# Kernel optimization log

Hardware: AMD Instinct MI355X
Metric: run time of the kernel (lower is better)

The kernel has to match this reference:

```python
import jax, jax.numpy as jnp
import numpy as np
from jax import lax

P_LEN, Q_LEN, B = 400, 60, 128
P_IN, Q_IN, H = 512, 512, 256
D = P_IN + Q_IN  # gate / GRU input size


def setup_inputs() -> dict:
    key = jax.random.key(0)
    ks = jax.random.split(key, 10)
    s = 0.05  # small init scale to keep tanh/sigmoid in sane range
    return {
        "q_input": jax.random.normal(ks[0], (Q_LEN, B, Q_IN), jnp.float32),
        "p_input": jax.random.normal(ks[1], (P_LEN, B, P_IN), jnp.float32),
        "q_mask": jnp.zeros((Q_LEN, B), dtype=bool),
        "Wq": jax.random.normal(ks[2], (2, Q_IN, H), jnp.float32) * s,
        "Wp": jax.random.normal(ks[3], (2, P_IN, H), jnp.float32) * s,
        "Ws": jax.random.normal(ks[4], (2, H, H), jnp.float32) * s,
        "v": jax.random.normal(ks[5], (2, H, 1), jnp.float32) * s,
        "gate_W": jax.random.normal(ks[6], (2, D, D), jnp.float32) * s,
        "gate_b": jnp.zeros((2, D), jnp.float32),
        "gru_Wih": jax.random.normal(ks[7], (2, 3 * H, D), jnp.float32) * s,
        "gru_Whh": jax.random.normal(ks[8], (2, 3 * H, H), jnp.float32) * s,
        "gru_bih": jnp.zeros((2, 3 * H), jnp.float32),
        "gru_bhh": jnp.zeros((2, 3 * H), jnp.float32),
    }


def _run_direction(q_input, p_input, q_mask, Wq, Wp, Ws, v,
                   gate_W, gate_b, gru_Wih, gru_Whh, gru_bih, gru_bhh,
                   reverse):
    # q_input: [Q, B, q_in], p_input: [P, B, p_in], q_mask: [Q, B] bool
    hid = Ws.shape[1]
    q_temp = jnp.einsum('qbe,eh->qbh', q_input, Wq)  # precomputed once, [Q,B,H]
    p_temp = jnp.einsum('pbe,eh->pbh', p_input, Wp)  # [P,B,H]
    mask = q_mask[:, :, None]                        # [Q,B,1]

    def step(state, xs):
        p_x, p_t = xs  # [B,p_in], [B,H]
        state_temp = state @ Ws                                   # [B,H]
        logits = jnp.tanh(q_temp + p_t[None] + state_temp[None]) @ v  # [Q,B,1]
        logits = jnp.where(mask, -jnp.inf, logits)
        weights = jax.nn.softmax(logits, axis=0)                  # over q_len
        att = jnp.sum(weights * q_input, axis=0)                  # [B,q_in]
        x = jnp.concatenate([p_x, att], axis=-1)                  # [B,D]
        x = x * jax.nn.sigmoid(x @ gate_W.T + gate_b)             # Gate
        # torch GRUCell math
        gi = x @ gru_Wih.T + gru_bih
        gh = state @ gru_Whh.T + gru_bhh
        i_r, i_z, i_n = jnp.split(gi, 3, axis=-1)
        h_r, h_z, h_n = jnp.split(gh, 3, axis=-1)
        r = jax.nn.sigmoid(i_r + h_r)
        z = jax.nn.sigmoid(i_z + h_z)
        n = jnp.tanh(i_n + r * h_n)
        new_state = (1.0 - z) * n + z * state
        return new_state, new_state

    init = jnp.zeros((p_input.shape[1], hid), p_input.dtype)
    _, out = lax.scan(step, init, (p_input, p_temp), reverse=reverse)
    return out  # [P,B,H], already in original time order (scan reverse handles it)


def reference(q_input, p_input, q_mask, Wq, Wp, Ws, v, gate_W, gate_b,
              gru_Wih, gru_Whh, gru_bih, gru_bhh):
    out_fw = _run_direction(q_input, p_input, q_mask, Wq[0], Wp[0], Ws[0], v[0],
                            gate_W[0], gate_b[0], gru_Wih[0], gru_Whh[0],
                            gru_bih[0], gru_bhh[0], reverse=False)
    out_bw = _run_direction(q_input, p_input, q_mask, Wq[1], Wp[1], Ws[1], v[1],
                            gate_W[1], gate_b[1], gru_Wih[1], gru_Whh[1],
                            gru_bih[1], gru_bhh[1], reverse=True)
    return jnp.concatenate([out_fw, out_bw], axis=-1)  # [P,B,2H]
```

## Files before the change

### kernel.cpp

```cpp
#include <hip/hip_runtime.h>

#define PL 400
#define QL 60
#define BB 128
#define EE 512
#define HH 256
#define DD 1024
#define G3 768
#define NBLK 256
#define NTHR 512
#define LDK 72

typedef __attribute__((ext_vector_type(8))) short bfrag;
typedef __attribute__((ext_vector_type(4))) float facc;
typedef __attribute__((ext_vector_type(4))) unsigned uintx4;
typedef __attribute__((ext_vector_type(4))) unsigned short ushortx4;

__device__ __forceinline__ unsigned short f2bf(float x) {
  unsigned u = __float_as_uint(x);
  return (unsigned short)((u + 0x7fffu + ((u >> 16) & 1u)) >> 16);
}
__device__ __forceinline__ float bf2f(unsigned short h) {
  return __uint_as_float(((unsigned)h) << 16);
}
__device__ __forceinline__ void split_bf(float x, unsigned short& hi, unsigned short& lo) {
  hi = f2bf(x);
  lo = f2bf(x - bf2f(hi));
}
__device__ __forceinline__ unsigned packf(float x) {
  unsigned short hi, lo;
  split_bf(x, hi, lo);
  return ((unsigned)hi << 16) | lo;
}
__device__ __forceinline__ float unpk(unsigned p) {
  return bf2f((unsigned short)(p >> 16)) + bf2f((unsigned short)(p & 0xffffu));
}
__device__ __forceinline__ float sigm(float x) {
  return __builtin_amdgcn_rcpf(1.f + __expf(-x));
}
__device__ __forceinline__ float ftanh(float x) {
  float xc = fminf(fmaxf(x, -10.f), 10.f);
  float t = __expf(2.f * xc);
  return (t - 1.f) * __builtin_amdgcn_rcpf(t + 1.f);
}

__device__ __forceinline__ float ald(const float* p) {
  return __hip_atomic_load((float*)p, __ATOMIC_RELAXED, __HIP_MEMORY_SCOPE_AGENT);
}
__device__ __forceinline__ void ast(float* p, float v) {
  __hip_atomic_store(p, v, __ATOMIC_RELAXED, __HIP_MEMORY_SCOPE_AGENT);
}
__device__ __forceinline__ unsigned aldu(const unsigned* p) {
  return __hip_atomic_load((unsigned*)p, __ATOMIC_RELAXED, __HIP_MEMORY_SCOPE_AGENT);
}
__device__ __forceinline__ void astu(unsigned* p, unsigned v) {
  __hip_atomic_store(p, v, __ATOMIC_RELAXED, __HIP_MEMORY_SCOPE_AGENT);
}
__device__ __forceinline__ unsigned long long aldull(const unsigned long long* p) {
  return __hip_atomic_load((unsigned long long*)p, __ATOMIC_RELAXED, __HIP_MEMORY_SCOPE_AGENT);
}
__device__ __forceinline__ void pollge(unsigned* f, unsigned tgt) {
  unsigned sp = 0;
  while (aldu(f) < tgt) {
    __builtin_amdgcn_s_sleep(1);
    if (++sp > (1u << 26)) break;
  }
}

constexpr size_t SZ_PT  = (size_t)2 * PL * BB * HH;
constexpr size_t SZ_GIP = (size_t)2 * 4 * BB * G3;
constexpr size_t SZ_GHP = (size_t)2 * BB * G3;
constexpr size_t SZ_WST = (size_t)2 * HH * HH;
constexpr size_t OFF_PT  = 0;
constexpr size_t OFF_GIP = OFF_PT + SZ_PT;
constexpr size_t OFF_GHP = OFF_GIP + SZ_GIP;
constexpr size_t OFF_WST = OFF_GHP + SZ_GHP;
constexpr size_t F32_TOT = OFF_WST + SZ_WST;
constexpr size_t UOFF_ATTP  = 0;
constexpr size_t UOFF_XPACK = UOFF_ATTP + (size_t)2 * 2 * BB * EE;
constexpr size_t UOFF_HPACK = UOFF_XPACK + (size_t)2 * 2 * BB * DD;
constexpr size_t U_TOT      = UOFF_HPACK + (size_t)2 * BB * HH;
constexpr size_t HSZ_WQT = (size_t)2 * HH * EE;
constexpr size_t HSZ_GW  = (size_t)2 * DD * DD;
constexpr size_t HSZ_WIH = (size_t)2 * G3 * DD;
constexpr size_t HSZ_WHH = (size_t)2 * G3 * HH;
constexpr size_t HOFF_WQTH = 0;
constexpr size_t HOFF_WQTL = HOFF_WQTH + HSZ_WQT;
constexpr size_t HOFF_WPTH = HOFF_WQTL + HSZ_WQT;
constexpr size_t HOFF_WPTL = HOFF_WPTH + HSZ_WQT;
constexpr size_t HOFF_GWH  = HOFF_WPTL + HSZ_WQT;
constexpr size_t HOFF_GWL  = HOFF_GWH + HSZ_GW;
constexpr size_t HOFF_WIHH = HOFF_GWL + HSZ_GW;
constexpr size_t HOFF_WIHL = HOFF_WIHH + HSZ_WIH;
constexpr size_t HOFF_WHHH = HOFF_WIHL + HSZ_WIH;
constexpr size_t HOFF_WHHL = HOFF_WHHH + HSZ_WHH;
constexpr size_t HOFF_QIN16 = HOFF_WHHL + HSZ_WHH;
constexpr size_t HOFF_QT16  = HOFF_QIN16 + (size_t)QL * BB * EE;
constexpr size_t H_TOT      = HOFF_QT16 + (size_t)2 * QL * BB * HH;

#define FA 0
#define FG 256
#define FI 320
#define FH 416
#define FC 440

__device__ __forceinline__ void gbar(unsigned* slots, unsigned gen) {
  asm volatile("" ::: "memory");
  __syncthreads();
  if (threadIdx.x == 0)
    __hip_atomic_store(&slots[blockIdx.x], gen, __ATOMIC_RELAXED, __HIP_MEMORY_SCOPE_AGENT);
  if (threadIdx.x < NBLK) pollge(&slots[threadIdx.x], gen);
  __syncthreads();
  asm volatile("" ::: "memory");
}

template <int NT, bool BSPLIT, int NCH, int ASRC>
__device__ void gemm_direct(facc* acc,
                            const unsigned short* wh, const unsigned short* wl,
                            const unsigned* apk, const float* a32, int as,
                            int kbase, int wchbase) {
  const int tid = threadIdx.x;
  const int lane = tid & 63;
  const int w = tid >> 6;
  constexpr int FN = NT / 16;
  const int lr = lane & 15;
  const int lk = (lane >> 4) << 3;
  const int row = (w << 4) + lr;

#pragma unroll 2
  for (int ch = 0; ch < NCH; ++ch) {
    const int kk = kbase + (ch << 6);
#pragma unroll
    for (int k32 = 0; k32 < 64; k32 += 32) {
      const int ko = kk + k32 + lk;
      bfrag ah, al_;
      {
        unsigned hu[4], lu[4];
        if constexpr (ASRC == 0) {
          const unsigned long long* src =
              (const unsigned long long*)(apk + (size_t)row * as + ko);
          unsigned long long d0 = aldull(src + 0);
          unsigned long long d1 = aldull(src + 1);
          unsigned long long d2 = aldull(src + 2);
          unsigned long long d3 = aldull(src + 3);
          unsigned p0 = (unsigned)d0, p1 = (unsigned)(d0 >> 32);
          unsigned p2 = (unsigned)d1, p3 = (unsigned)(d1 >> 32);
          unsigned p4 = (unsigned)d2, p5 = (unsigned)(d2 >> 32);
          unsigned p6 = (unsigned)d3, p7 = (unsigned)(d3 >> 32);
          hu[0] = (p0 >> 16) | (p1 & 0xffff0000u);  lu[0] = (p0 & 0xffffu) | (p1 << 16);
          hu[1] = (p2 >> 16) | (p3 & 0xffff0000u);  lu[1] = (p2 & 0xffffu) | (p3 << 16);
          hu[2] = (p4 >> 16) | (p5 & 0xffff0000u);  lu[2] = (p4 & 0xffffu) | (p5 << 16);
          hu[3] = (p6 >> 16) | (p7 & 0xffff0000u);  lu[3] = (p6 & 0xffffu) | (p7 << 16);
        } else {
          const float* src = a32 + (size_t)row * as + ko;
          float4 v0 = *(const float4*)src;
          float4 v1 = *(const float4*)(src + 4);
          unsigned short h0, l0, h1, l1;
          split_bf(v0.x, h0, l0); split_bf(v0.y, h1, l1);
          hu[0] = h0 | ((unsigned)h1 << 16); lu[0] = l0 | ((unsigned)l1 << 16);
          split_bf(v0.z, h0, l0); split_bf(v0.w, h1, l1);
          hu[1] = h0 | ((unsigned)h1 << 16); lu[1] = l0 | ((unsigned)l1 << 16);
          split_bf(v1.x, h0, l0); split_bf(v1.y, h1, l1);
          hu[2] = h0 | ((unsigned)h1 << 16); lu[2] = l0 | ((unsigned)l1 << 16);
          split_bf(v1.z, h0, l0); split_bf(v1.w, h1, l1);
          hu[3] = h0 | ((unsigned)h1 << 16); lu[3] = l0 | ((unsigned)l1 << 16);
        }
        uintx4 hv = {hu[0], hu[1], hu[2], hu[3]};
        uintx4 lv = {lu[0], lu[1], lu[2], lu[3]};
        ah  = __builtin_bit_cast(bfrag, hv);
        al_ = __builtin_bit_cast(bfrag, lv);
      }
      bfrag bhf[FN], blf[FN];
#pragma unroll
      for (int f = 0; f < FN; f++) {
        const int bo = ((wchbase + ch) * NT + (f << 4) + lr) * LDK + k32 + lk;
        bhf[f] = *(const bfrag*)&wh[bo];
        if constexpr (BSPLIT) blf[f] = *(const bfrag*)&wl[bo];
      }
#pragma unroll
      for (int j = 0; j < FN; j++) {
        acc[j] = __builtin_amdgcn_mfma_f32_16x16x32_bf16(al_, bhf[j], acc[j], 0, 0, 0);
        if constexpr (BSPLIT)
          acc[j] = __builtin_amdgcn_mfma_f32_16x16x32_bf16(ah, blf[j], acc[j], 0, 0, 0);
        acc[j] = __builtin_amdgcn_mfma_f32_16x16x32_bf16(ah, bhf[j], acc[j], 0, 0, 0);
      }
    }
  }
}

__device__ void gemm_pro(unsigned short* sAh, unsigned short* sAl, unsigned short* warea,
                         const float* a32,
                         const unsigned short* bh_g, const unsigned short* bl_g,
                         float* dstf, unsigned short* dst16) {
  const int tid = threadIdx.x;
  const int lane = tid & 63;
  const int w = tid >> 6;
  const int wm = (w >> 2) << 6;
  const int wn = (w & 3) << 5;
  const int lr = lane & 15;
  const int lk = (lane >> 4) << 3;
  unsigned short* wh = warea;
  unsigned short* wl = warea + 128 * LDK;
  const facc fz = {0.f, 0.f, 0.f, 0.f};
  facc acc[4][2];
#pragma unroll
  for (int i = 0; i < 4; i++)
#pragma unroll
    for (int j = 0; j < 2; j++) acc[i][j] = fz;
  for (int ch = 0; ch < 8; ++ch) {
    const int kk0 = ch << 6;
    for (int i = tid; i < 8192; i += NTHR) {
      const int r = i >> 6, k = i & 63;
      unsigned short uh, ul;
      split_bf(a32[(size_t)r * EE + kk0 + k], uh, ul);
      sAh[r * LDK + k] = uh;
      sAl[r * LDK + k] = ul;
      wh[r * LDK + k] = bh_g[(size_t)r * EE + kk0 + k];
      wl[r * LDK + k] = bl_g[(size_t)r * EE + kk0 + k];
    }
    __syncthreads();
#pragma unroll
    for (int k32 = 0; k32 < 64; k32 += 32) {
      bfrag ah[4], al_[4], bhf[2], blf[2];
#pragma unroll
      for (int f = 0; f < 4; f++) {
        const int ao = (wm + (f << 4) + lr) * LDK + k32 + lk;
        ah[f]  = *(const bfrag*)&sAh[ao];
        al_[f] = *(const bfrag*)&sAl[ao];
      }
#pragma unroll
      for (int f = 0; f < 2; f++) {
        const int bo = (wn + (f << 4) + lr) * LDK + k32 + lk;
        bhf[f] = *(const bfrag*)&wh[bo];
        blf[f] = *(const bfrag*)&wl[bo];
      }
#pragma unroll
      for (int i = 0; i < 4; i++)
#pragma unroll
        for (int j = 0; j < 2; j++) {
          acc[i][j] = __builtin_amdgcn_mfma_f32_16x16x32_bf16(al_[i], bhf[j], acc[i][j], 0, 0, 0);
          acc[i][j] = __builtin_amdgcn_mfma_f32_16x16x32_bf16(ah[i], blf[j], acc[i][j], 0, 0, 0);
          acc[i][j] = __builtin_amdgcn_mfma_f32_16x16x32_bf16(ah[i], bhf[j], acc[i][j], 0, 0, 0);
        }
    }
    __syncthreads();
  }
  const int orow = (lane >> 4) << 2;
  const int ocol = lane & 15;
#pragma unroll
  for (int i = 0; i < 4; i++)
#pragma unroll
    for (int j = 0; j < 2; j++)
#pragma unroll
      for (int q = 0; q < 4; q++) {
        const size_t o = (size_t)(wm + (i << 4) + orow + q) * HH + (wn + (j << 4) + ocol);
        if (dstf) dstf[o] = acc[i][j][q];
        else dst16[o] = f2bf(acc[i][j][q]);
      }
}

__global__ void __launch_bounds__(256) k_transpose_qp(
    const float* __restrict__ Wq, const float* __restrict__ Wp,
    unsigned short* __restrict__ wqth, unsigned short* __restrict__ wqtl,
    unsigned short* __restrict__ wpth, unsigned short* __restrict__ wptl) {
  __shared__ float tile[64 * 65];
  const int blk = blockIdx.x;
  const int mat = blk >> 6;
  const int rem = blk & 63;
  const int d = rem >> 5;
  const int rem2 = rem & 31;
  const int kt = rem2 >> 2;
  const int nt = rem2 & 3;
  const float* src = mat ? Wp : Wq;
  unsigned short* dh = mat ? wpth : wqth;
  unsigned short* dl = mat ? wptl : wqtl;
  const int tid = threadIdx.x;
  for (int i = tid; i < 4096; i += 256) {
    int kr = i >> 6, nc = i & 63;
    tile[kr * 65 + nc] = src[((size_t)d * EE + kt * 64 + kr) * HH + nt * 64 + nc];
  }
  __syncthreads();
  for (int i = tid; i < 4096; i += 256) {
    int n = i >> 6, k = i & 63;
    unsigned short hi, lo;
    split_bf(tile[k * 65 + n], hi, lo);
    size_t o = ((size_t)d * HH + nt * 64 + n) * EE + kt * 64 + k;
    dh[o] = hi; dl[o] = lo;
  }
}

__global__ void __launch_bounds__(256) k_split_w(
    const float* __restrict__ gw, const float* __restrict__ wih, const float* __restrict__ whh,
    unsigned short* __restrict__ gwh, unsigned short* __restrict__ gwl,
    unsigned short* __restrict__ wihh, unsigned short* __restrict__ wihl,
    unsigned short* __restrict__ whhh, unsigned short* __restrict__ whhl) {
  const size_t N1 = HSZ_GW, N2 = HSZ_WIH, N3 = HSZ_WHH;
  for (size_t i = (size_t)blockIdx.x * 256 + threadIdx.x; i < N1 + N2 + N3;
       i += (size_t)gridDim.x * 256) {
    float x; unsigned short *ph, *pl; size_t o;
    if (i < N1)           { o = i;           x = gw[o];  ph = gwh;  pl = gwl; }
    else if (i < N1 + N2) { o = i - N1;      x = wih[o]; ph = wihh; pl = wihl; }
    else                  { o = i - N1 - N2; x = whh[o]; ph = whhh; pl = whhl; }
    unsigned short hi, lo;
    split_bf(x, hi, lo);
    ph[o] = hi; pl[o] = lo;
  }
}

__global__ void __launch_bounds__(256) k_wst_qin(const float* __restrict__ Ws,
                                                 float* __restrict__ wst,
                                                 const float* __restrict__ qin,
                                                 unsigned short* __restrict__ qin16) {
  const size_t NQ = (size_t)QL * BB * EE;
  for (size_t i = (size_t)blockIdx.x * 256 + threadIdx.x; i < SZ_WST + NQ;
       i += (size_t)gridDim.x * 256) {
    if (i < SZ_WST) {
      int d = (int)(i >> 16);
      int j = (int)((i >> 8) & 255);
      int k = (int)(i & 255);
      wst[i] = Ws[((size_t)d * HH + k) * HH + j];
    } else {
      size_t o = i - SZ_WST;
      qin16[o] = f2bf(qin[o]);
    }
  }
}

__global__ void __launch_bounds__(NTHR, 1) pe_main(
    const float* __restrict__ qin, const float* __restrict__ pin,
    const unsigned char* __restrict__ qmask,
    const float* __restrict__ vvec, const float* __restrict__ gateb,
    const float* __restrict__ bih, const float* __restrict__ bhh,
    float* __restrict__ out,
    float* __restrict__ fws, unsigned* __restrict__ upck,
    unsigned short* __restrict__ hws, unsigned* __restrict__ bar) {
  __shared__ __align__(16) unsigned short smem[56320];
  unsigned short* sAh = smem;
  unsigned short* sAl = smem + 9216;
  unsigned short* warea = smem + 18432;
  float* fsm = (float*)smem;
  float* sv_perm   = (float*)(smem + 55296);
  float* sstv_perm = (float*)(smem + 55808);

  float* pt   = fws + OFF_PT;
  float* gip  = fws + OFF_GIP;
  float* ghp  = fws + OFF_GHP;
  float* wst  = fws + OFF_WST;
  unsigned* attp0 = upck + UOFF_ATTP;
  unsigned* xpck0 = upck + UOFF_XPACK;
  unsigned* hpack = upck + UOFF_HPACK;
  unsigned short* wqth = hws + HOFF_WQTH;
  unsigned short* wqtl = hws + HOFF_WQTL;
  unsigned short* wpth = hws + HOFF_WPTH;
  unsigned short* wptl = hws + HOFF_WPTL;
  unsigned short* gwh  = hws + HOFF_GWH;
  unsigned short* wihh = hws + HOFF_WIHH;
  unsigned short* wihl = hws + HOFF_WIHL;
  unsigned short* whhh = hws + HOFF_WHHH;
  unsigned short* whhl = hws + HOFF_WHHL;
  const unsigned short* qin16 = hws + HOFF_QIN16;
  unsigned short* qt16 = hws + HOFF_QT16;
  unsigned* flg = bar + 256;

  const int blk = blockIdx.x;
  const int tid = threadIdx.x;
  const int lane = tid & 63;
  const int w = tid >> 6;

  const bool isGate = (blk < 64);
  const bool isGi   = (blk >= 64 && blk < 160);
  const bool isGh   = (blk >= 160 && blk < 184);
  const int gd = blk >> 5, gct = blk & 31, coloff = gct * 32;
  const int gi_g = blk - 64, id_ = gi_g / 48, ir = gi_g % 48;
  const int int_ = ir >> 2, iks = ir & 3;
  const int gh_g = blk - 160, hd = gh_g / 12, hnt = gh_g % 12;

  for (int tt = blk; tt < 1840; tt += NBLK) {
    if (tt < 1600) {
      int d = tt / 800, rem = tt % 800, mt = rem >> 1, ntp = rem & 1;
      gemm_pro(sAh, sAl, warea, pin + (size_t)mt * BB * EE,
               wpth + ((size_t)d * HH + ntp * 128) * EE,
               wptl + ((size_t)d * HH + ntp * 128) * EE,
               pt + ((size_t)d * PL * BB + (size_t)mt * BB) * HH + ntp * 128, nullptr);
    } else {
      int u2 = tt - 1600;
      int d = u2 / 120, rem = u2 % 120, mt = rem >> 1, ntp = rem & 1;
      gemm_pro(sAh, sAl, warea, qin + (size_t)mt * BB * EE,
               wqth + ((size_t)d * HH + ntp * 128) * EE,
               wqtl + ((size_t)d * HH + ntp * 128) * EE,
               nullptr,
               qt16 + ((size_t)d * QL * BB + (size_t)mt * BB) * HH + ntp * 128);
    }
  }

  if (isGate) {
    const unsigned short* src = gwh + (size_t)(gd * DD + coloff) * DD;
    for (int i = tid; i < 32768; i += NTHR) {
      int ch = i >> 11, n = (i >> 6) & 31, k = i & 63;
      warea[(ch * 32 + n) * LDK + k] = src[(size_t)n * DD + ch * 64 + k];
    }
  } else if (isGi) {
    const unsigned short* sh = wihh + (size_t)(id_ * G3 + int_ * 64) * DD + iks * 256;
    const unsigned short* sl = wihl + (size_t)(id_ * G3 + int_ * 64) * DD + iks * 256;
    for (int i = tid; i < 16384; i += NTHR) {
      int ch = i >> 12, n = (i >> 6) & 63, k = i & 63;
      warea[(ch * 64 + n) * LDK + k]         = sh[(size_t)n * DD + ch * 64 + k];
      warea[18432 + (ch * 64 + n) * LDK + k] = sl[(size_t)n * DD + ch * 64 + k];
    }
  } else if (isGh) {
    const unsigned short* sh = whhh + (size_t)(hd * G3 + hnt * 64) * HH;
    const unsigned short* sl = whhl + (size_t)(hd * G3 + hnt * 64) * HH;
    for (int i = tid; i < 16384; i += NTHR) {
      int ch = i >> 12, n = (i >> 6) & 63, k = i & 63;
      warea[(ch * 64 + n) * LDK + k]         = sh[(size_t)n * HH + ch * 64 + k];
      warea[18432 + (ch * 64 + n) * LDK + k] = sl[(size_t)n * HH + ch * 64 + k];
    }
  }

  __builtin_amdgcn_fence(__ATOMIC_RELEASE, "agent");
  gbar(bar, 1);

  const int d_ab = blk >> 7, b_ab = blk & 127;
  if (tid < 256) {
    sv_perm[tid] = vvec[d_ab * HH + tid];
    sstv_perm[tid] = 0.f;
  }
  const bool qmv = (tid < 64 && lane < QL) ? (qmask[lane * BB + b_ab] != 0) : false;
  __syncthreads();

  facc pinacc[2];
  if (isGate) {
    const facc fz = {0.f, 0.f, 0.f, 0.f};
    pinacc[0] = fz; pinacc[1] = fz;
    const int t0 = gd ? (PL - 1) : 0;
    gemm_direct<32, false, 8, 1>(pinacc, warea, nullptr,
                                 nullptr, pin + (size_t)t0 * BB * EE, EE, 0, 0);
  }

  float hreg = 0.f;
  float* sm = fsm;
  float* slog = fsm + 512;
  float* swgt = fsm + 576;
  float* spart = fsm + 896;
  float* hrow = fsm + 1408;

  for (int s = 0; s < PL; ++s) {
    const int par = s & 1;
    unsigned* attp = attp0 + (size_t)par * 2 * BB * EE;
    unsigned* xpack = xpck0 + (size_t)par * 2 * BB * DD;
    const unsigned gen = (unsigned)(s + 1);

    {
      const int d = d_ab, b = b_ab;
      const int t = d ? (PL - 1 - s) : s;
      if (tid < 256) {
        float ptv = __builtin_nontemporal_load(&pt[(((size_t)d * PL + t) * BB + b) * HH + tid]);
        sm[tid] = sstv_perm[tid] + ptv;
      }
      __syncthreads();
      {
        const int j4 = lane << 2;
        const float4 smv = *(const float4*)&sm[j4];
        const float4 svv = *(const float4*)&sv_perm[j4];
        for (int q = w; q < QL; q += 8) {
          const unsigned short* qrow = qt16 + (((size_t)d * QL + q) * BB + b) * HH;
          ushortx4 qv = *(const ushortx4*)&qrow[j4];
          float a = ftanh(bf2f(qv.x) + smv.x) * svv.x
                  + ftanh(bf2f(qv.y) + smv.y) * svv.y
                  + ftanh(bf2f(qv.z) + smv.z) * svv.z
                  + ftanh(bf2f(qv.w) + smv.w) * svv.w;
          for (int off = 32; off; off >>= 1) a += __shfl_down(a, off, 64);
          if (lane == 0) slog[q] = a;
        }
      }
      __syncthreads();
      if (tid < 64) {
        float x = -3.0e38f;
        if (lane < QL) {
          x = slog[lane];
          if (qmv) x = -3.0e38f;
        }
        float mx = x;
        for (int off = 32; off; off >>= 1) mx = fmaxf(mx, __shfl_xor(mx, off, 64));
        float e = (lane < QL) ? __expf(x - mx) : 0.f;
        float sum2 = e;
        for (int off = 32; off; off >>= 1) sum2 += __shfl_xor(sum2, off, 64);
        if (lane < QL) swgt[lane] = e * __builtin_amdgcn_rcpf(sum2);
      }
      __syncthreads();
      {
        const int c = tid;
        float a0 = 0.f, a1 = 0.f, a2 = 0.f, a3 = 0.f;
        const unsigned short* qb = qin16 + (size_t)b * EE + c;
        for (int q = 0; q < QL; q += 4) {
          a0 += swgt[q]     * bf2f(qb[(size_t)q * BB * EE]);
          a1 += swgt[q + 1] * bf2f(qb[(size_t)(q + 1) * BB * EE]);
          a2 += swgt[q + 2] * bf2f(qb[(size_t)(q + 2) * BB * EE]);
          a3 += swgt[q + 3] * bf2f(qb[(size_t)(q + 3) * BB * EE]);
        }
        astu(&attp[((size_t)d * BB + b) * EE + c], packf((a0 + a1) + (a2 + a3)));
      }
      __syncthreads();
      if (tid == 0) astu(&flg[FA + d_ab * 128 + b_ab], gen);
    }

    const int orow = (lane >> 4) << 2;
    const int ocol = lane & 15;
    const int rbase = w << 4;

    if (isGate) {
      if (tid < 128) pollge(&flg[FA + gd * 128 + tid], gen);
      __syncthreads();
      gemm_direct<32, false, 8, 0>(pinacc, warea, nullptr,
                                   attp + (size_t)gd * BB * EE, nullptr, EE, 0, 8);
      {
        const int t = gd ? (PL - 1 - s) : s;
        const float* pin_t = pin + (size_t)t * BB * EE;
#pragma unroll
        for (int i = 0; i < 2; i++)
#pragma unroll
          for (int q = 0; q < 4; q++) {
            const int row = rbase + orow + q;
            const int gcol = coloff + (i << 4) + ocol;
            float uv = (gct < 16) ? pin_t[(size_t)row * EE + gcol]
                                  : unpk(aldu(&attp[((size_t)gd * BB + row) * EE + gcol - EE]));
            float x = uv * sigm(pinacc[i][q] + gateb[(size_t)gd * DD + gcol]);
            astu(&xpack[((size_t)gd * BB + row) * DD + gcol], packf(x));
          }
      }
      __syncthreads();
      if (tid == 0) astu(&flg[FG + gd * 32 + gct], gen);
      if (s + 1 < PL) {
        const facc fz = {0.f, 0.f, 0.f, 0.f};
        pinacc[0] = fz; pinacc[1] = fz;
        const int t2 = gd ? (PL - 2 - s) : (s + 1);
        gemm_direct<32, false, 8, 1>(pinacc, warea, nullptr,
                                     nullptr, pin + (size_t)t2 * BB * EE, EE, 0, 0);
      }
    } else if (isGi) {
      if (tid < 8) pollge(&flg[FG + id_ * 32 + iks * 8 + tid], gen);
      __syncthreads();
      const facc fz = {0.f, 0.f, 0.f, 0.f};
      facc acc[4] = {fz, fz, fz, fz};
      gemm_direct<64, true, 4, 0>(acc, warea, warea + 18432,
                                  xpack + (size_t)id_ * BB * DD, nullptr, DD, iks * 256, 0);
#pragma unroll
      for (int j = 0; j < 4; j++)
#pragma unroll
        for (int q = 0; q < 4; q++) {
          const int row = rbase + orow + q;
          const int col = int_ * 64 + (j << 4) + ocol;
          ast(&gip[((size_t)(id_ * 4 + iks) * BB + row) * G3 + col], acc[j][q]);
        }
      __syncthreads();
      if (tid == 0) astu(&flg[FI + id_ * 48 + ir], gen);
    } else if (isGh) {
      if (s > 0 && tid < 128) pollge(&flg[FC + hd * 128 + tid], (unsigned)s);
      __syncthreads();
      const facc fz = {0.f, 0.f, 0.f, 0.f};
      facc acc[4] = {fz, fz, fz, fz};
      gemm_direct<64, true, 4, 0>(acc, warea, warea + 18432,
                                  hpack + (size_t)hd * BB * HH, nullptr, HH, 0, 0);
#pragma unroll
      for (int j = 0; j < 4; j++)
#pragma unroll
        for (int q = 0; q < 4; q++) {
          const int row = rbase + orow + q;
          const int col = hnt * 64 + (j << 4) + ocol;
          ast(&ghp[((size_t)hd * BB + row) * G3 + col], acc[j][q]);
        }
      __syncthreads();
      if (tid == 0) astu(&flg[FH + hd * 12 + hnt], gen);
    }

    {
      if (tid < 48) pollge(&flg[FI + d_ab * 48 + tid], gen);
      else if (tid < 60) pollge(&flg[FH + d_ab * 12 + (tid - 48)], gen);
      __syncthreads();
      const int d = d_ab, b = b_ab;
      const int j = tid & 255, half = tid >> 8;
      const int t = d ? (PL - 1 - s) : s;
      const size_t rb = (size_t)d * BB + b;
      float gi3[3], gh3[3];
#pragma unroll
      for (int c3 = 0; c3 < 3; c3++) {
        float acc2 = bih[(size_t)d * G3 + c3 * HH + j];
#pragma unroll
        for (int ks = 0; ks < 4; ks++)
          acc2 += ald(&gip[((size_t)(d * 4 + ks) * BB + b) * G3 + c3 * HH + j]);
        gi3[c3] = acc2;
        gh3[c3] = ald(&ghp[rb * G3 + c3 * HH + j]) + bhh[(size_t)d * G3 + c3 * HH + j];
      }
      float r = sigm(gi3[0] + gh3[0]);
      float z = sigm(gi3[1] + gh3[1]);
      float n = ftanh(gi3[2] + r * gh3[2]);
      float hn = (1.f - z) * n + z * hreg;
      hreg = hn;
      if (half == 0) {
        __builtin_nontemporal_store(hn, &out[((size_t)t * BB + b) * 512 + d * HH + j]);
        astu(&hpack[rb * HH + j], packf(hn));
        hrow[j] = hn;
      }
      __syncthreads();
      if (tid == 0) astu(&flg[FC + d_ab * 128 + b_ab], gen);
      float part = 0.f;
      const float* wr = wst + ((size_t)d * HH + j) * HH + (half << 7);
      const float* hr = hrow + (half << 7);
#pragma unroll
      for (int k = 0; k < 128; k += 4) {
        float4 w4 = *(const float4*)&wr[k];
        float4 h4 = *(const float4*)&hr[k];
        part += w4.x * h4.x + w4.y * h4.y + w4.z * h4.z + w4.w * h4.w;
      }
      spart[tid] = part;
      __syncthreads();
      if (tid < 256) sstv_perm[tid] = spart[tid] + spart[tid + 256];
      __syncthreads();
    }
  }
}

extern "C" void kernel_launch(void* const* d_in, const int* in_sizes, int n_in,
                              void* d_out, int out_size, void* d_ws, size_t ws_size,
                              hipStream_t stream) {
  const float* qin = (const float*)d_in[0];
  const float* pin = (const float*)d_in[1];
  const unsigned char* qmask = (const unsigned char*)d_in[2];
  const float* Wq  = (const float*)d_in[3];
  const float* Wp  = (const float*)d_in[4];
  const float* Ws  = (const float*)d_in[5];
  const float* v   = (const float*)d_in[6];
  const float* gw  = (const float*)d_in[7];
  const float* gb  = (const float*)d_in[8];
  const float* wih = (const float*)d_in[9];
  const float* whh = (const float*)d_in[10];
  const float* bih = (const float*)d_in[11];
  const float* bhh = (const float*)d_in[12];
  float* out = (float*)d_out;

  char* base = (char*)d_ws;
  float* fws = (float*)base;
  unsigned* upck = (unsigned*)(base + F32_TOT * sizeof(float));
  unsigned short* hws = (unsigned short*)(base + F32_TOT * sizeof(float) + U_TOT * sizeof(unsigned));
  unsigned* bar = (unsigned*)(base + F32_TOT * sizeof(float) + U_TOT * sizeof(unsigned) +
                              H_TOT * sizeof(unsigned short));
  size_t need = F32_TOT * sizeof(float) + U_TOT * sizeof(unsigned) +
                H_TOT * sizeof(unsigned short) + 8192;
  if (ws_size < need) return;

  hipMemsetAsync(upck + UOFF_HPACK, 0, (size_t)2 * BB * HH * sizeof(unsigned), stream);
  hipMemsetAsync(bar, 0, 4096, stream);

  k_transpose_qp<<<128, 256, 0, stream>>>(Wq, Wp,
      hws + HOFF_WQTH, hws + HOFF_WQTL, hws + HOFF_WPTH, hws + HOFF_WPTL);
  k_split_w<<<1024, 256, 0, stream>>>(gw, wih, whh,
      hws + HOFF_GWH, hws + HOFF_GWL, hws + HOFF_WIHH, hws + HOFF_WIHL,
      hws + HOFF_WHHH, hws + HOFF_WHHL);
  k_wst_qin<<<2048, 256, 0, stream>>>(Ws, fws + OFF_WST, qin,
                                      hws + HOFF_QIN16);
  pe_main<<<NBLK, NTHR, 0, stream>>>(qin, pin, qmask, v, gb, bih, bhh, out,
                                     fws, upck, hws, bar);
}
```

Measured before the change: 24.87 ms.

## Drop A-low MFMA pass in gate GEMM and cache q_temp slice in LDS

Adds an ASPLIT template flag so the gate GEMM uses only the bf16-high part of the activation. This removes one of the two MFMAs per fragment plus the low-part unpacking, while the GI/GH GEMMs keep full split precision. It also copies each block's q_temp slice (QL x H bf16) into extra LDS once, so the per-step attention logits read it from shared memory instead of global memory. Gate accuracy drops somewhat, and the larger LDS footprint could matter for occupancy, though there is only one block per CU here.

```diff
diff --git a/kernel.cpp b/kernel.cpp
--- a/kernel.cpp
+++ b/kernel.cpp
@@ -114,7 +114,7 @@
   asm volatile("" ::: "memory");
 }
 
-template <int NT, bool BSPLIT, int NCH, int ASRC>
+template <int NT, bool BSPLIT, int NCH, int ASRC, bool ASPLIT>
 __device__ void gemm_direct(facc* acc,
                             const unsigned short* wh, const unsigned short* wl,
                             const unsigned* apk, const float* a32, int as,
@@ -147,28 +147,43 @@
           unsigned p2 = (unsigned)d1, p3 = (unsigned)(d1 >> 32);
           unsigned p4 = (unsigned)d2, p5 = (unsigned)(d2 >> 32);
           unsigned p6 = (unsigned)d3, p7 = (unsigned)(d3 >> 32);
-          hu[0] = (p0 >> 16) | (p1 & 0xffff0000u);  lu[0] = (p0 & 0xffffu) | (p1 << 16);
-          hu[1] = (p2 >> 16) | (p3 & 0xffff0000u);  lu[1] = (p2 & 0xffffu) | (p3 << 16);
-          hu[2] = (p4 >> 16) | (p5 & 0xffff0000u);  lu[2] = (p4 & 0xffffu) | (p5 << 16);
-          hu[3] = (p6 >> 16) | (p7 & 0xffff0000u);  lu[3] = (p6 & 0xffffu) | (p7 << 16);
+          hu[0] = (p0 >> 16) | (p1 & 0xffff0000u);
+          hu[1] = (p2 >> 16) | (p3 & 0xffff0000u);
+          hu[2] = (p4 >> 16) | (p5 & 0xffff0000u);
+          hu[3] = (p6 >> 16) | (p7 & 0xffff0000u);
+          if constexpr (ASPLIT) {
+            lu[0] = (p0 & 0xffffu) | (p1 << 16);
+            lu[1] = (p2 & 0xffffu) | (p3 << 16);
+            lu[2] = (p4 & 0xffffu) | (p5 << 16);
+            lu[3] = (p6 & 0xffffu) | (p7 << 16);
+          }
         } else {
           const float* src = a32 + (size_t)row * as + ko;
           float4 v0 = *(const float4*)src;
           float4 v1 = *(const float4*)(src + 4);
-          unsigned short h0, l0, h1, l1;
-          split_bf(v0.x, h0, l0); split_bf(v0.y, h1, l1);
-          hu[0] = h0 | ((unsigned)h1 << 16); lu[0] = l0 | ((unsigned)l1 << 16);
-          split_bf(v0.z, h0, l0); split_bf(v0.w, h1, l1);
-          hu[1] = h0 | ((unsigned)h1 << 16); lu[1] = l0 | ((unsigned)l1 << 16);
-          split_bf(v1.x, h0, l0); split_bf(v1.y, h1, l1);
-          hu[2] = h0 | ((unsigned)h1 << 16); lu[2] = l0 | ((unsigned)l1 << 16);
-          split_bf(v1.z, h0, l0); split_bf(v1.w, h1, l1);
-          hu[3] = h0 | ((unsigned)h1 << 16); lu[3] = l0 | ((unsigned)l1 << 16);
+          if constexpr (ASPLIT) {
+            unsigned short h0, l0, h1, l1;
+            split_bf(v0.x, h0, l0); split_bf(v0.y, h1, l1);
+            hu[0] = h0 | ((unsigned)h1 << 16); lu[0] = l0 | ((unsigned)l1 << 16);
+            split_bf(v0.z, h0, l0); split_bf(v0.w, h1, l1);
+            hu[1] = h0 | ((unsigned)h1 << 16); lu[1] = l0 | ((unsigned)l1 << 16);
+            split_bf(v1.x, h0, l0); split_bf(v1.y, h1, l1);
+            hu[2] = h0 | ((unsigned)h1 << 16); lu[2] = l0 | ((unsigned)l1 << 16);
+            split_bf(v1.z, h0, l0); split_bf(v1.w, h1, l1);
+            hu[3] = h0 | ((unsigned)h1 << 16); lu[3] = l0 | ((unsigned)l1 << 16);
+          } else {
+            hu[0] = f2bf(v0.x) | ((unsigned)f2bf(v0.y) << 16);
+            hu[1] = f2bf(v0.z) | ((unsigned)f2bf(v0.w) << 16);
+            hu[2] = f2bf(v1.x) | ((unsigned)f2bf(v1.y) << 16);
+            hu[3] = f2bf(v1.z) | ((unsigned)f2bf(v1.w) << 16);
+          }
         }
         uintx4 hv = {hu[0], hu[1], hu[2], hu[3]};
-        uintx4 lv = {lu[0], lu[1], lu[2], lu[3]};
-        ah  = __builtin_bit_cast(bfrag, hv);
-        al_ = __builtin_bit_cast(bfrag, lv);
+        ah = __builtin_bit_cast(bfrag, hv);
+        if constexpr (ASPLIT) {
+          uintx4 lv = {lu[0], lu[1], lu[2], lu[3]};
+          al_ = __builtin_bit_cast(bfrag, lv);
+        }
       }
       bfrag bhf[FN], blf[FN];
 #pragma unroll
@@ -179,7 +194,8 @@
       }
 #pragma unroll
       for (int j = 0; j < FN; j++) {
-        acc[j] = __builtin_amdgcn_mfma_f32_16x16x32_bf16(al_, bhf[j], acc[j], 0, 0, 0);
+        if constexpr (ASPLIT)
+          acc[j] = __builtin_amdgcn_mfma_f32_16x16x32_bf16(al_, bhf[j], acc[j], 0, 0, 0);
         if constexpr (BSPLIT)
           acc[j] = __builtin_amdgcn_mfma_f32_16x16x32_bf16(ah, blf[j], acc[j], 0, 0, 0);
         acc[j] = __builtin_amdgcn_mfma_f32_16x16x32_bf16(ah, bhf[j], acc[j], 0, 0, 0);
@@ -334,13 +350,14 @@
     float* __restrict__ out,
     float* __restrict__ fws, unsigned* __restrict__ upck,
     unsigned short* __restrict__ hws, unsigned* __restrict__ bar) {
-  __shared__ __align__(16) unsigned short smem[56320];
+  __shared__ __align__(16) unsigned short smem[71680];
   unsigned short* sAh = smem;
   unsigned short* sAl = smem + 9216;
   unsigned short* warea = smem + 18432;
   float* fsm = (float*)smem;
   float* sv_perm   = (float*)(smem + 55296);
   float* sstv_perm = (float*)(smem + 55808);
+  unsigned short* qt_lds = smem + 56320;
 
   float* pt   = fws + OFF_PT;
   float* gip  = fws + OFF_GIP;
@@ -425,6 +442,10 @@
     sv_perm[tid] = vvec[d_ab * HH + tid];
     sstv_perm[tid] = 0.f;
   }
+  for (int i = tid; i < QL * HH; i += NTHR) {
+    const int q = i >> 8, j = i & 255;
+    qt_lds[i] = qt16[(((size_t)d_ab * QL + q) * BB + b_ab) * HH + j];
+  }
   const bool qmv = (tid < 64 && lane < QL) ? (qmask[lane * BB + b_ab] != 0) : false;
   __syncthreads();
 
@@ -433,8 +454,8 @@
     const facc fz = {0.f, 0.f, 0.f, 0.f};
     pinacc[0] = fz; pinacc[1] = fz;
     const int t0 = gd ? (PL - 1) : 0;
-    gemm_direct<32, false, 8, 1>(pinacc, warea, nullptr,
-                                 nullptr, pin + (size_t)t0 * BB * EE, EE, 0, 0);
+    gemm_direct<32, false, 8, 1, false>(pinacc, warea, nullptr,
+                                        nullptr, pin + (size_t)t0 * BB * EE, EE, 0, 0);
   }
 
   float hreg = 0.f;
@@ -463,8 +484,7 @@
         const float4 smv = *(const float4*)&sm[j4];
         const float4 svv = *(const float4*)&sv_perm[j4];
         for (int q = w; q < QL; q += 8) {
-          const unsigned short* qrow = qt16 + (((size_t)d * QL + q) * BB + b) * HH;
-          ushortx4 qv = *(const ushortx4*)&qrow[j4];
+          ushortx4 qv = *(const ushortx4*)&qt_lds[q * HH + j4];
           float a = ftanh(bf2f(qv.x) + smv.x) * svv.x
                   + ftanh(bf2f(qv.y) + smv.y) * svv.y
                   + ftanh(bf2f(qv.z) + smv.z) * svv.z
@@ -511,8 +531,8 @@
     if (isGate) {
       if (tid < 128) pollge(&flg[FA + gd * 128 + tid], gen);
       __syncthreads();
-      gemm_direct<32, false, 8, 0>(pinacc, warea, nullptr,
-                                   attp + (size_t)gd * BB * EE, nullptr, EE, 0, 8);
+      gemm_direct<32, false, 8, 0, false>(pinacc, warea, nullptr,
+                                          attp + (size_t)gd * BB * EE, nullptr, EE, 0, 8);
       {
         const int t = gd ? (PL - 1 - s) : s;
         const float* pin_t = pin + (size_t)t * BB * EE;
@@ -534,16 +554,17 @@
         const facc fz = {0.f, 0.f, 0.f, 0.f};
         pinacc[0] = fz; pinacc[1] = fz;
         const int t2 = gd ? (PL - 2 - s) : (s + 1);
-        gemm_direct<32, false, 8, 1>(pinacc, warea, nullptr,
-                                     nullptr, pin + (size_t)t2 * BB * EE, EE, 0, 0);
+        gemm_direct<32, false, 8, 1, false>(pinacc, warea, nullptr,
+                                            nullptr, pin + (size_t)t2 * BB * EE, EE, 0, 0);
       }
     } else if (isGi) {
       if (tid < 8) pollge(&flg[FG + id_ * 32 + iks * 8 + tid], gen);
       __syncthreads();
       const facc fz = {0.f, 0.f, 0.f, 0.f};
       facc acc[4] = {fz, fz, fz, fz};
-      gemm_direct<64, true, 4, 0>(acc, warea, warea + 18432,
-                                  xpack + (size_t)id_ * BB * DD, nullptr, DD, iks * 256, 0);
+      gemm_direct<64, true, 4, 0, true>(acc, warea, warea + 18432,
+                                        xpack + (size_t)id_ * BB * DD, nullptr, DD,
+                                        iks * 256, 0);
 #pragma unroll
       for (int j = 0; j < 4; j++)
 #pragma unroll
@@ -559,8 +580,8 @@
       __syncthreads();
       const facc fz = {0.f, 0.f, 0.f, 0.f};
       facc acc[4] = {fz, fz, fz, fz};
-      gemm_direct<64, true, 4, 0>(acc, warea, warea + 18432,
-                                  hpack + (size_t)hd * BB * HH, nullptr, HH, 0, 0);
+      gemm_direct<64, true, 4, 0, true>(acc, warea, warea + 18432,
+                                        hpack + (size_t)hd * BB * HH, nullptr, HH, 0, 0);
 #pragma unroll
       for (int j = 0; j < 4; j++)
 #pragma unroll
```

After: 24.52 ms. No clear change (-1.4%).
